# Kernel optimization log

Measured on AMD Instinct MI355X. Metric: run time of the kernel, lower is better.

The kernel has to match this reference:

```python
import jax, jax.numpy as jnp
import numpy as np

C = 768
HEADS = 12
NF = 8      # num_frames
SL = 196    # seq_len (patches per frame)
B = 2
N = 1 + NF * SL
HID = 4 * C


def _ln(x, g, b, eps=1e-5):
    mu = jnp.mean(x, axis=-1, keepdims=True)
    var = jnp.mean((x - mu) ** 2, axis=-1, keepdims=True)
    return (x - mu) * jax.lax.rsqrt(var + eps) * g + b


def setup_inputs() -> dict:
    key = jax.random.key(0)
    ks = jax.random.split(key, 16)
    s = 0.02
    return {
        "x": jax.random.normal(ks[0], (B, N, C), jnp.float32),
        "g1": jnp.ones((C,), jnp.float32),
        "b1": jnp.zeros((C,), jnp.float32),
        "Wqkv": jax.random.normal(ks[1], (C, 3 * C), jnp.float32) * s,
        "Wq": jax.random.normal(ks[2], (C, C), jnp.float32) * s,
        "Wkv": jax.random.normal(ks[3], (C, 2 * C), jnp.float32) * s,
        "Wp": jax.random.normal(ks[4], (C, C), jnp.float32) * s,
        "bp": jnp.zeros((C,), jnp.float32),
        "g2": jnp.ones((C,), jnp.float32),
        "b2": jnp.zeros((C,), jnp.float32),
        "W1": jax.random.normal(ks[5], (C, HID), jnp.float32) * s,
        "bf1": jnp.zeros((HID,), jnp.float32),
        "W2": jax.random.normal(ks[6], (HID, C), jnp.float32) * s,
        "bf2": jnp.zeros((C,), jnp.float32),
        "seq_len": SL,
        "num_frames": NF,
    }


def _traj_attn(xn, Wqkv, Wq, Wkv, Wp, bp, P, F):
    Bb, Nn, Cc = xn.shape
    h = HEADS
    d = Cc // h
    scale = d ** -0.5
    S = F * P  # non-cls tokens

    qkv = xn @ Wqkv                                   # (B,N,3C)
    q, k, v = jnp.split(qkv, 3, axis=-1)

    def heads(t):  # (B,N,C) -> (B*h, N, d)
        return t.reshape(Bb, Nn, h, d).transpose(0, 2, 1, 3).reshape(Bb * h, Nn, d)

    q, k, v = heads(q), heads(k), heads(v)
    cls_q, q_ = q[:, :1], q[:, 1:]
    k_ = k[:, 1:]
    v_ = v[:, 1:]

    # cls token attends to all tokens
    sim = jnp.einsum('bid,bjd->bij', cls_q * scale, k)
    cls_out = jnp.einsum('bij,bjd->bid', jax.nn.softmax(sim, axis=-1), v)
    cls_out = cls_out.reshape(Bb, h, 1, d).transpose(0, 2, 1, 3).reshape(Bb, 1, Cc)

    # stage 1: space-only softmax per frame
    qk = jnp.einsum('bqd,bkd->bqk', q_, k_).reshape(Bb * h, S, F, P)
    space_attn = jax.nn.softmax(scale * qk, axis=-1)          # (Bh,S,F,P)
    v_r = v_.reshape(Bb * h, F, P, d)
    x1 = jnp.einsum('bqfn,bfnd->bqfd', space_attn, v_r)       # (Bh,S,F,d)
    x1 = x1.reshape(Bb, h, S, F, d).transpose(0, 2, 3, 1, 4).reshape(Bb, S, F, Cc)

    # diagonal across (query-frame, key-frame)
    xg = x1.reshape(Bb, F, P, F, Cc)
    diag = jnp.diagonal(xg, axis1=1, axis2=3)                 # (B,P,C,F)
    x_diag = diag.transpose(0, 3, 1, 2).reshape(Bb, S, Cc)    # b (f n) d

    # stage 2: frame-wise attention
    q2 = (x_diag @ Wq).reshape(Bb, S, h, d).transpose(0, 2, 1, 3) * scale  # bhsd
    kv2 = x1 @ Wkv
    k2, v2 = jnp.split(kv2, 2, axis=-1)
    k2 = k2.reshape(Bb, S, F, h, d).transpose(0, 3, 1, 2, 4)  # bhsfd
    attn2 = jax.nn.softmax(jnp.einsum('bhsd,bhsfd->bhsf', q2, k2), axis=-1)
    xo = x1.reshape(Bb, S, F, h, d).transpose(0, 3, 1, 2, 4)  # use_original_code=True
    out = jnp.einsum('bhsf,bhsfd->bhsd', attn2, xo)
    out = out.transpose(0, 2, 1, 3).reshape(Bb, S, Cc)

    out = jnp.concatenate([cls_out, out], axis=1) @ Wp + bp
    return out


def reference(x, g1, b1, Wqkv, Wq, Wkv, Wp, bp, g2, b2, W1, bf1, W2, bf2, seq_len, num_frames):
    x = x + _traj_attn(_ln(x, g1, b1), Wqkv, Wq, Wkv, Wp, bp, seq_len, num_frames)
    h = _ln(x, g2, b2)
    h = jax.nn.gelu(h @ W1 + bf1, approximate=False) @ W2 + bf2
    return x + h
```

## Files before the change

kernel.cpp:

```cpp
#include <hip/hip_runtime.h>
#include <hip/hip_bf16.h>
#include <math.h>

#define C     768
#define HEADS 12
#define HD    64
#define NF    8
#define SL    196
#define BB    2
#define NN    1569
#define SS    1568
#define HID   3072
#define CLS_CH 256
#define CLS_NC 7
#define QSCALE 0.18033688011112042f

typedef __attribute__((ext_vector_type(8))) short short8;
typedef __attribute__((ext_vector_type(4))) float f32x4;
typedef unsigned short u16;

__device__ inline float fast_exp2(float x) { return __builtin_amdgcn_exp2f(x); }

__device__ inline u16 f2b(float f) {
    __hip_bfloat16 h = __float2bfloat16(f);
    return *reinterpret_cast<u16*>(&h);
}
__device__ inline float b2f(u16 u) {
    union { unsigned u; float f; } v; v.u = ((unsigned)u) << 16;
    return v.f;
}

__device__ inline void gload_lds16(const void* g, void* l) {
    __builtin_amdgcn_global_load_lds(
        (const __attribute__((address_space(1))) void*)g,
        (__attribute__((address_space(3))) void*)l, 16, 0, 0);
}

__global__ void ln_kernel(const float* __restrict__ x, const float* __restrict__ g,
                          const float* __restrict__ b, u16* __restrict__ out, int rows) {
    int row = blockIdx.x;
    if (row >= rows) return;
    const float* xr = x + (size_t)row * C;
    int tid = threadIdx.x;
    float v[3];
    float sum = 0.f, sumsq = 0.f;
#pragma unroll
    for (int i = 0; i < 3; i++) {
        v[i] = xr[tid + 256 * i];
        sum += v[i]; sumsq += v[i] * v[i];
    }
    __shared__ float s1[4], s2[4];
    for (int off = 32; off; off >>= 1) {
        sum   += __shfl_xor(sum, off);
        sumsq += __shfl_xor(sumsq, off);
    }
    int wave = tid >> 6, lane = tid & 63;
    if (lane == 0) { s1[wave] = sum; s2[wave] = sumsq; }
    __syncthreads();
    sum   = s1[0] + s1[1] + s1[2] + s1[3];
    sumsq = s2[0] + s2[1] + s2[2] + s2[3];
    float mu  = sum / C;
    float var = sumsq / C - mu * mu;
    float rstd = rsqrtf(fmaxf(var, 0.f) + 1e-5f);
    u16* outr = out + (size_t)row * C;
#pragma unroll
    for (int i = 0; i < 3; i++) {
        int c = tid + 256 * i;
        outr[c] = f2b((v[i] - mu) * rstd * g[c] + b[c]);
    }
}

__global__ void wtrans_all_kernel(
    const float* __restrict__ Wqkv, const float* __restrict__ Wq,
    const float* __restrict__ Wkv,  const float* __restrict__ Wp,
    const float* __restrict__ W1,   const float* __restrict__ W2,
    u16* Tqkv, u16* Tq, u16* Tkv, u16* Tp, u16* T1, u16* T2) {
    __shared__ float tile[64][65];
    int bid = blockIdx.x;
    const float* W; u16* Wt; int K, ldb, gx;
    if (bid < 432)       { W = Wqkv; Wt = Tqkv; K = 768;  ldb = 2304; gx = 36; }
    else if (bid < 576)  { W = Wq;   Wt = Tq;   K = 768;  ldb = 768;  gx = 12; bid -= 432; }
    else if (bid < 720)  { W = Wkv;  Wt = Tkv;  K = 768;  ldb = 1536; gx = 12; bid -= 576; }
    else if (bid < 864)  { W = Wp;   Wt = Tp;   K = 768;  ldb = 768;  gx = 12; bid -= 720; }
    else if (bid < 1440) { W = W1;   Wt = T1;   K = 768;  ldb = 3072; gx = 48; bid -= 864; }
    else                 { W = W2;   Wt = T2;   K = 3072; ldb = 768;  gx = 12; bid -= 1440; }
    int nb = (bid % gx) * 64, kb = (bid / gx) * 64;
    int tx = threadIdx.x & 63, ty = threadIdx.x >> 6;
#pragma unroll
    for (int i = 0; i < 64; i += 4)
        tile[ty + i][tx] = W[(size_t)(kb + ty + i) * ldb + nb + tx];
    __syncthreads();
#pragma unroll
    for (int i = 0; i < 64; i += 4)
        Wt[(size_t)(nb + ty + i) * K + kb + tx] = f2b(tile[tx][ty + i]);
}

template<int MODE, int BM, int BN>
__global__ __launch_bounds__(256) void gemm_bf16(
    const u16* __restrict__ A, const u16* __restrict__ Bt,
    const float* __restrict__ bias, const float* resid, void* Cout,
    int M, int N, int K, int lda, int ldb, int gx) {
    constexpr int MT   = BM / 32;
    constexpr int NT   = BN / 32;
    constexpr int ACH  = BM * 4;
    constexpr int TCH  = (BM + BN) * 4;
    constexpr int HALF = (BM + BN) * 64;
    __shared__ char smem[2 * HALF];
    int tid = threadIdx.x, lane = tid & 63, wave = tid >> 6;
    int wr = wave >> 1, wc = wave & 1;
    int r16 = lane & 15, kg = lane >> 4;

    int nwg = gridDim.x, orig = blockIdx.x;
    int qq = nwg >> 3, rr = nwg & 7, xcd = orig & 7, lid = orig >> 3;
    int wg = (xcd < rr ? xcd * (qq + 1) : rr * (qq + 1) + (xcd - rr) * qq) + lid;
    int bx = wg % gx, by = wg / gx;
    if constexpr (MODE == 4) {
        int mt_ = (M + BM - 1) / BM;
        int chunk = by / mt_; by -= chunk * mt_;
        A    += (size_t)chunk * K;
        Bt   += (size_t)chunk * K;
        Cout  = (void*)((float*)Cout + (size_t)chunk * ((size_t)M * N));
    }
    int row0 = by * BM, col0 = bx * BN;

    f32x4 acc[MT][NT];
#pragma unroll
    for (int mt = 0; mt < MT; mt++)
#pragma unroll
        for (int nt = 0; nt < NT; nt++) acc[mt][nt] = (f32x4){0.f, 0.f, 0.f, 0.f};

    auto stage = [&](char* dstbase, int ks) {
        int k0 = ks << 5;
#pragma unroll
        for (int it = 0; it < TCH / 256; it++) {
            int c = it * 256 + tid;
            const u16* src;
            if (c < ACH) {
                int ml = c >> 2, s = c & 3;
                int kgs = s ^ ((ml >> 1) & 3);
                int gm = row0 + ml; if (gm >= M) gm = M - 1;
                src = A + (size_t)gm * lda + k0 + kgs * 8;
            } else {
                int cc = c - ACH;
                int nl = cc >> 2, s = cc & 3;
                int kgs = s ^ ((nl >> 1) & 3);
                src = Bt + (size_t)(col0 + nl) * ldb + k0 + kgs * 8;
            }
            gload_lds16(src, dstbase + it * 4096 + wave * 1024);
        }
    };

    int nsteps = K >> 5;
    stage(smem, 0);
    __syncthreads();
    for (int ks = 0; ks < nsteps; ks++) {
        char* curb = smem + (ks & 1) * HALF;
        if (ks + 1 < nsteps) stage(smem + ((ks + 1) & 1) * HALF, ks + 1);
        short8 af[MT], bfr[NT];
#pragma unroll
        for (int mt = 0; mt < MT; mt++) {
            int ml = wr * (BM / 2) + mt * 16 + r16;
            af[mt] = *(const short8*)(curb + ml * 64 + ((kg ^ ((ml >> 1) & 3)) << 4));
        }
#pragma unroll
        for (int nt = 0; nt < NT; nt++) {
            int nl = wc * (BN / 2) + nt * 16 + r16;
            bfr[nt] = *(const short8*)(curb + BM * 64 + nl * 64 + ((kg ^ ((nl >> 1) & 3)) << 4));
        }
        __builtin_amdgcn_s_setprio(1);
#pragma unroll
        for (int mt = 0; mt < MT; mt++)
#pragma unroll
            for (int nt = 0; nt < NT; nt++)
                acc[mt][nt] = __builtin_amdgcn_mfma_f32_16x16x32_bf16(af[mt], bfr[nt], acc[mt][nt], 0, 0, 0);
        __builtin_amdgcn_s_setprio(0);
        __syncthreads();
    }
#pragma unroll
    for (int mt = 0; mt < MT; mt++) {
#pragma unroll
        for (int r2 = 0; r2 < 4; r2++) {
            int gm = row0 + wr * (BM / 2) + mt * 16 + kg * 4 + r2;
            if (gm >= M) continue;
#pragma unroll
            for (int nt = 0; nt < NT; nt++) {
                int gn = col0 + wc * (BN / 2) + nt * 16 + r16;
                float v = acc[mt][nt][r2];
                if constexpr (MODE == 1) {
                    v += bias[gn];
                    v = 0.5f * v * (1.f + erff(v * 0.70710678118f));
                }
                if constexpr (MODE == 2) {
                    v += bias[gn] + resid[(size_t)gm * N + gn];
                    ((float*)Cout)[(size_t)gm * N + gn] = v;
                } else if constexpr (MODE == 4) {
                    ((float*)Cout)[(size_t)gm * N + gn] = v;
                } else {
                    if constexpr (MODE == 3) { if (gn < 768) v *= QSCALE; }
                    ((u16*)Cout)[(size_t)gm * N + gn] = f2b(v);
                }
            }
        }
    }
}

__global__ void fc2_merge_kernel(const float* __restrict__ p,
                                 const float* __restrict__ bias, float* __restrict__ out) {
    int i = blockIdx.x * 256 + threadIdx.x;
    int total = BB * NN * (C / 4);
    if (i >= total) return;
    int c4 = i % (C / 4);
    size_t stride = (size_t)BB * NN * (C / 4);
    float4 bb = ((const float4*)bias)[c4];
    float4 a0 = ((const float4*)p)[i];
    float4 a1 = ((const float4*)p)[i + stride];
    float4 a2 = ((const float4*)p)[i + 2 * stride];
    float4 a3 = ((const float4*)p)[i + 3 * stride];
    float4 o  = ((float4*)out)[i];
    o.x += a0.x + a1.x + a2.x + a3.x + bb.x;
    o.y += a0.y + a1.y + a2.y + a3.y + bb.y;
    o.z += a0.z + a1.z + a2.z + a3.z + bb.z;
    o.w += a0.w + a1.w + a2.w + a3.w + bb.w;
    ((float4*)out)[i] = o;
}

__global__ void cls_partial_kernel(const u16* __restrict__ qkv, float* __restrict__ part) {
    int c = blockIdx.x, bh = blockIdx.y;
    int b = bh / HEADS, hh = bh % HEADS;
    int tid = threadIdx.x;
    int wave = tid >> 6, lane = tid & 63;
    __shared__ float s_q[HD];
    __shared__ float s_sc[CLS_CH];
    __shared__ float sm[4], ss[4];
    __shared__ float sacc[4][HD];
    if (tid < HD) s_q[tid] = b2f(qkv[(size_t)(b * NN) * 2304 + hh * HD + tid]);
    __syncthreads();

    int j0 = c * CLS_CH;
    int j = j0 + tid;
    float sc = -1e30f;
    if (j < NN) {
        const short8* kp = (const short8*)(qkv + ((size_t)(b * NN) + j) * 2304 + C + hh * HD);
        float acc = 0.f;
#pragma unroll
        for (int u = 0; u < 8; u++) {
            short8 kv = kp[u];
#pragma unroll
            for (int e = 0; e < 8; e++) acc += s_q[u * 8 + e] * b2f((u16)kv[e]);
        }
        sc = acc;
    }
    float m = sc;
    for (int off = 32; off; off >>= 1) m = fmaxf(m, __shfl_xor(m, off));
    if (lane == 0) sm[wave] = m;
    __syncthreads();
    m = fmaxf(fmaxf(sm[0], sm[1]), fmaxf(sm[2], sm[3]));
    float e = (j < NN) ? fast_exp2(sc - m) : 0.f;
    s_sc[tid] = e;
    float su = e;
    for (int off = 32; off; off >>= 1) su += __shfl_xor(su, off);
    if (lane == 0) ss[wave] = su;
    __syncthreads();
    float ssum = ss[0] + ss[1] + ss[2] + ss[3];

    int jj = tid >> 6, d = tid & 63;
    int jmax = NN - j0; if (jmax > CLS_CH) jmax = CLS_CH;
    const u16* vcol = qkv + ((size_t)(b * NN) + j0) * 2304 + 2 * C + hh * HD + d;
    float acc = 0.f;
    for (int t = jj; t < jmax; t += 4)
        acc += s_sc[t] * b2f(vcol[(size_t)t * 2304]);
    sacc[jj][d] = acc;
    __syncthreads();
    if (tid < HD) {
        float pv = sacc[0][tid] + sacc[1][tid] + sacc[2][tid] + sacc[3][tid];
        float* pp = part + ((size_t)bh * CLS_NC + c) * 66;
        pp[2 + tid] = pv;
        if (tid == 0) { pp[0] = m; pp[1] = ssum; }
    }
}

__global__ void cls_reduce_kernel(const float* __restrict__ part, u16* __restrict__ y) {
    int bh = blockIdx.x;
    int b = bh / HEADS, hh = bh % HEADS;
    int d = threadIdx.x;
    float gm = -1e30f;
#pragma unroll
    for (int c = 0; c < CLS_NC; c++)
        gm = fmaxf(gm, part[((size_t)bh * CLS_NC + c) * 66]);
    float tot = 0.f, pv = 0.f;
#pragma unroll
    for (int c = 0; c < CLS_NC; c++) {
        const float* pp = part + ((size_t)bh * CLS_NC + c) * 66;
        float w = fast_exp2(pp[0] - gm);
        tot += pp[1] * w;
        pv  += pp[2 + d] * w;
    }
    y[(size_t)(b * NN) * C + hh * HD + d] = f2b(pv / tot);
}

__global__ void repack_kv_kernel(const u16* __restrict__ qkv,
                                 u16* __restrict__ Kb, u16* __restrict__ Vt) {
    const int NK = 24 * NF * 208 * 8;
    const int NV = 24 * NF * 64 * 28;
    int t = blockIdx.x * 256 + threadIdx.x;
    if (t < NK) {
        int d8 = t & 7;
        int rest = t >> 3;
        int n = rest % 208;
        rest /= 208;
        int f = rest % NF;
        int bh = rest / NF;
        int b = bh / HEADS, h = bh % HEADS;
        short8 v = {0, 0, 0, 0, 0, 0, 0, 0};
        if (n < SL)
            v = *(const short8*)(qkv + ((size_t)(b * NN) + 1 + f * SL + n) * 2304 + C + h * HD + d8 * 8);
        *(short8*)(Kb + (((size_t)bh * NF + f) * 208 + n) * 64 + d8 * 8) = v;
    } else {
        int u = t - NK;
        if (u >= NV) return;
        int n8 = u % 28;
        int rest = u / 28;
        int d = rest % 64;
        rest /= 64;
        int f = rest % NF;
        int bh = rest / NF;
        int b = bh / HEADS, h = bh % HEADS;
        int n0 = n8 * 8;
        const u16* src = qkv + ((size_t)(b * NN) + 1 + f * SL) * 2304 + 2 * C + h * HD + d;
        short8 v;
#pragma unroll
        for (int jj = 0; jj < 8; jj++) {
            int n = n0 + jj;
            v[jj] = (n < SL) ? (short)src[(size_t)n * 2304] : (short)0;
        }
        *(short8*)(Vt + (((size_t)bh * NF + f) * 64 + d) * 224 + n0) = v;
    }
}

__global__ void space_attn_mfma(
    const u16* __restrict__ qkv, const u16* __restrict__ Kb,
    const u16* __restrict__ Vt, u16* __restrict__ x1, u16* __restrict__ xd) {
    __shared__ u16 smem[14848];
    int tid = threadIdx.x;
    int lane = tid & 63, wave = tid >> 6;
    int r16 = lane & 15, kg = lane >> 4;

    int n = blockIdx.x;
    int xcd = n & 7;
    int slot = n >> 3;
    int j = slot % 25;
    int gw = slot / 25;
    int bh = xcd * 3 + gw % 3;
    int f = gw / 3;
    int b = bh / HEADS, h = bh % HEADS;

    int strip = j * 4 + wave;
    bool act = strip < 98;
    if (!act) strip = 97;
    int q0 = strip * 16;

    const u16* qrow = qkv + ((size_t)(b * NN) + 1 + q0 + r16) * 2304 + h * HD + kg * 8;
    short8 aq0 = *(const short8*)(qrow);
    short8 aq1 = *(const short8*)(qrow + 32);

    const char* kb_g = (const char*)(Kb + ((size_t)bh * NF + f) * 208 * 64);
    for (int w = wave; w < 26; w += 4) {
        int p = w * 1024 + lane * 16;
        int row = p >> 7;
        int src = (p & ~127) | ((p & 127) ^ ((row & 7) << 4));
        gload_lds16(kb_g + src, (char*)smem + p);
    }
    __syncthreads();

    f32x4 acc[13];
#pragma unroll
    for (int t = 0; t < 13; t++) acc[t] = (f32x4){0.f, 0.f, 0.f, 0.f};
    const char* ksm = (const char*)smem;
    int swz = (r16 & 7) << 4;
    __builtin_amdgcn_s_setprio(1);
#pragma unroll
    for (int t = 0; t < 13; t++) {
        const char* krow = ksm + (t * 16 + r16) * 128;
        short8 bk0 = *(const short8*)(krow + ((kg * 16) ^ swz));
        short8 bk1 = *(const short8*)(krow + ((64 + kg * 16) ^ swz));
        acc[t] = __builtin_amdgcn_mfma_f32_16x16x32_bf16(aq0, bk0, acc[t], 0, 0, 0);
        acc[t] = __builtin_amdgcn_mfma_f32_16x16x32_bf16(aq1, bk1, acc[t], 0, 0, 0);
    }
    __builtin_amdgcn_s_setprio(0);

    const u16* vbase = Vt + ((size_t)bh * NF + f) * 64 * 224;
    short8 vf[2][4];
#pragma unroll
    for (int dt = 0; dt < 4; dt++)
        vf[0][dt] = *(const short8*)(vbase + (dt * 16 + r16) * 224 + kg * 8);

    __syncthreads();
    u16* pb = smem + wave * 3712;

    bool tail_mask = (r16 >= 4);
    float ssum[4] = {0.f, 0.f, 0.f, 0.f};
#pragma unroll
    for (int t = 0; t < 13; t++) {
#pragma unroll
        for (int r = 0; r < 4; r++) {
            float p = (t == 12 && tail_mask) ? 0.f : fast_exp2(acc[t][r]);
            ssum[r] += p;
            pb[(kg * 4 + r) * 232 + t * 16 + r16] = f2b(p);
        }
    }
    {
        int zr = lane >> 2, zc = 208 + (lane & 3) * 4;
        *(uint2*)(&pb[zr * 232 + zc]) = (uint2){0u, 0u};
    }
#pragma unroll
    for (int off = 8; off; off >>= 1)
#pragma unroll
        for (int r = 0; r < 4; r++) ssum[r] += __shfl_xor(ssum[r], off);
    float inv[4];
#pragma unroll
    for (int r = 0; r < 4; r++) inv[r] = 1.f / ssum[r];

    f32x4 o[4];
#pragma unroll
    for (int dt = 0; dt < 4; dt++) o[dt] = (f32x4){0.f, 0.f, 0.f, 0.f};
    __builtin_amdgcn_s_setprio(1);
#pragma unroll
    for (int kc = 0; kc < 7; kc++) {
        if (kc < 6) {
#pragma unroll
            for (int dt = 0; dt < 4; dt++)
                vf[(kc + 1) & 1][dt] = *(const short8*)(vbase + (dt * 16 + r16) * 224 + (kc + 1) * 32 + kg * 8);
        }
        short8 pa = *(const short8*)(&pb[r16 * 232 + kc * 32 + kg * 8]);
#pragma unroll
        for (int dt = 0; dt < 4; dt++)
            o[dt] = __builtin_amdgcn_mfma_f32_16x16x32_bf16(pa, vf[kc & 1][dt], o[dt], 0, 0, 0);
    }
    __builtin_amdgcn_s_setprio(0);

    if (act) {
#pragma unroll
        for (int dt = 0; dt < 4; dt++)
#pragma unroll
            for (int r = 0; r < 4; r++)
                pb[(kg * 4 + r) * 72 + dt * 16 + r16] = f2b(o[dt][r] * inv[r]);
        u16* x1row = x1 + (((size_t)(b * SS + q0)) * NF + f) * C + h * HD;
        u16* xdrow = xd + ((size_t)(b * SS + q0)) * C + h * HD;
        int fbase = f * SL;
#pragma unroll
        for (int it = 0; it < 2; it++) {
            int c = it * 64 + lane;
            int qr = c >> 3, c8 = c & 7;
            short8 v8 = *(const short8*)(&pb[qr * 72 + c8 * 8]);
            *(short8*)(x1row + (size_t)qr * (NF * C) + c8 * 8) = v8;
            if ((unsigned)(q0 + qr - fbase) < (unsigned)SL)
                *(short8*)(xdrow + (size_t)qr * C + c8 * 8) = v8;
        }
    }
}

__global__ void attn2_kernel(const u16* __restrict__ q2, const u16* __restrict__ k2,
                             const u16* __restrict__ x1, u16* __restrict__ y) {
    int item = blockIdx.x * 4 + (threadIdx.x >> 6);
    if (item >= BB * HEADS * SS) return;
    int lane = threadIdx.x & 63;
    int s = item % SS;
    int bh = item / SS;
    int b = bh / HEADS, hh = bh % HEADS;
    size_t rowbs = (size_t)(b * SS + s);
    float qv = b2f(q2[rowbs * C + hh * HD + lane]) * QSCALE;
    float lg[NF];
#pragma unroll
    for (int f = 0; f < NF; f++) {
        float p = qv * b2f(k2[(rowbs * NF + f) * C + hh * HD + lane]);
        for (int off = 32; off; off >>= 1) p += __shfl_xor(p, off);
        lg[f] = p;
    }
    float m = lg[0];
#pragma unroll
    for (int f = 1; f < NF; f++) m = fmaxf(m, lg[f]);
    float sum = 0.f;
#pragma unroll
    for (int f = 0; f < NF; f++) { lg[f] = fast_exp2(lg[f] - m); sum += lg[f]; }
    float inv = 1.f / sum;
    float acc = 0.f;
#pragma unroll
    for (int f = 0; f < NF; f++) acc += lg[f] * b2f(x1[(rowbs * NF + f) * C + hh * HD + lane]);
    y[((size_t)(b * NN) + 1 + s) * C + hh * HD + lane] = f2b(acc * inv);
}

extern "C" void kernel_launch(void* const* d_in, const int* in_sizes, int n_in,
                              void* d_out, int out_size, void* d_ws, size_t ws_size,
                              hipStream_t stream) {
    const float* x    = (const float*)d_in[0];
    const float* g1   = (const float*)d_in[1];
    const float* b1   = (const float*)d_in[2];
    const float* Wqkv = (const float*)d_in[3];
    const float* Wq   = (const float*)d_in[4];
    const float* Wkv  = (const float*)d_in[5];
    const float* Wp   = (const float*)d_in[6];
    const float* bp   = (const float*)d_in[7];
    const float* g2   = (const float*)d_in[8];
    const float* b2_  = (const float*)d_in[9];
    const float* W1   = (const float*)d_in[10];
    const float* bf1  = (const float*)d_in[11];
    const float* W2   = (const float*)d_in[12];
    const float* bf2  = (const float*)d_in[13];
    float* out = (float*)d_out;

    u16* us     = (u16*)d_ws;
    u16* xn_b   = us;
    u16* qkv_b  = xn_b   + 2409984;
    u16* Wt_qkv = qkv_b  + 7229952;
    u16* Wt_q   = Wt_qkv + 1769472;
    u16* Wt_kv  = Wt_q   + 589824;
    u16* Wt_p   = Wt_kv  + 589824;
    u16* W1t    = Wt_p   + 589824;
    u16* W2t    = W1t    + 2359296;
    u16* Kb     = W2t    + 2359296;
    u16* Vt     = Kb     + 2555904;
    u16* x1b    = Vt     + 2752512;
    u16* xdb    = x1b    + 19267584;
    u16* q2b    = xdb    + 2408448;
    u16* k2b    = q2b    + 2408448;
    u16* y_b    = k2b    + 19267584;
    u16* a1b    = y_b    + 2409984;
    float* cls_ws   = (float*)(a1b + 9639936);
    float* fc2_part = cls_ws + 24 * 7 * 66;

    const int M1 = BB * NN;
    const int M2 = BB * SS;
    const int M3 = BB * SS * NF;

    wtrans_all_kernel<<<2016, 256, 0, stream>>>(Wqkv, Wq, Wkv, Wp, W1, W2,
                                                Wt_qkv, Wt_q, Wt_kv, Wt_p, W1t, W2t);
    ln_kernel<<<M1, 256, 0, stream>>>(x, g1, b1, xn_b, M1);
    gemm_bf16<3, 128, 64><<<36 * 25, 256, 0, stream>>>(
        xn_b, Wt_qkv, nullptr, nullptr, qkv_b, M1, 2304, 768, 768, 768, 36);
    repack_kv_kernel<<<(24 * NF * 208 * 8 + 24 * NF * 64 * 28 + 255) / 256, 256, 0, stream>>>(
        qkv_b, Kb, Vt);
    cls_partial_kernel<<<dim3(CLS_NC, BB * HEADS), 256, 0, stream>>>(qkv_b, cls_ws);
    cls_reduce_kernel<<<BB * HEADS, 64, 0, stream>>>(cls_ws, y_b);
    space_attn_mfma<<<4800, 256, 0, stream>>>(qkv_b, Kb, Vt, x1b, xdb);
    gemm_bf16<0, 64, 64><<<12 * 49, 256, 0, stream>>>(
        xdb, Wt_q, nullptr, nullptr, q2b, M2, 768, 768, 768, 768, 12);
    gemm_bf16<0, 128, 128><<<6 * 196, 256, 0, stream>>>(
        x1b, Wt_kv, nullptr, nullptr, k2b, M3, 768, 768, 768, 768, 6);
    attn2_kernel<<<(BB * HEADS * SS + 3) / 4, 256, 0, stream>>>(q2b, k2b, x1b, y_b);
    gemm_bf16<2, 64, 64><<<12 * 50, 256, 0, stream>>>(
        y_b, Wt_p, bp, x, out, M1, 768, 768, 768, 768, 12);
    ln_kernel<<<M1, 256, 0, stream>>>(out, g2, b2_, xn_b, M1);
    gemm_bf16<1, 128, 64><<<48 * 25, 256, 0, stream>>>(
        xn_b, W1t, bf1, nullptr, a1b, M1, 3072, 768, 768, 768, 48);
    gemm_bf16<4, 128, 64><<<12 * 25 * 4, 256, 0, stream>>>(
        a1b, W2t, nullptr, nullptr, fc2_part, M1, 768, 768, 3072, 3072, 12);
    fc2_merge_kernel<<<(BB * NN * (C / 4) + 255) / 256, 256, 0, stream>>>(
        fc2_part, bf2, out);
}
```

Before: 295.7 us.

## Transpose space-attn QK MFMA to store P row-contiguous; halve fc2 split-K

The space-attention kernel swaps the MFMA operand order so each lane holds scores for one query row across keys. This lets the row sum reduce with two cross-lane shuffles instead of per-register butterflies, and P is normalized before packed 8-byte stores to LDS instead of scattered 2-byte stores. Separately, the FC2 GEMM split-K factor drops from 4 to 2, so the merge kernel reads two partial buffers instead of four. The cost is fewer FC2 blocks for parallelism and more live registers for the stored exponentials.

```diff
diff --git a/kernel.cpp b/kernel.cpp
--- a/kernel.cpp
+++ b/kernel.cpp
@@ -18,6 +18,7 @@
 typedef __attribute__((ext_vector_type(8))) short short8;
 typedef __attribute__((ext_vector_type(4))) float f32x4;
 typedef unsigned short u16;
+typedef unsigned int u32;
 
 __device__ inline float fast_exp2(float x) { return __builtin_amdgcn_exp2f(x); }
 
@@ -214,13 +215,11 @@
     float4 bb = ((const float4*)bias)[c4];
     float4 a0 = ((const float4*)p)[i];
     float4 a1 = ((const float4*)p)[i + stride];
-    float4 a2 = ((const float4*)p)[i + 2 * stride];
-    float4 a3 = ((const float4*)p)[i + 3 * stride];
     float4 o  = ((float4*)out)[i];
-    o.x += a0.x + a1.x + a2.x + a3.x + bb.x;
-    o.y += a0.y + a1.y + a2.y + a3.y + bb.y;
-    o.z += a0.z + a1.z + a2.z + a3.z + bb.z;
-    o.w += a0.w + a1.w + a2.w + a3.w + bb.w;
+    o.x += a0.x + a1.x + bb.x;
+    o.y += a0.y + a1.y + bb.y;
+    o.z += a0.z + a1.z + bb.z;
+    o.w += a0.w + a1.w + bb.w;
     ((float4*)out)[i] = o;
 }
 
@@ -383,8 +382,8 @@
         const char* krow = ksm + (t * 16 + r16) * 128;
         short8 bk0 = *(const short8*)(krow + ((kg * 16) ^ swz));
         short8 bk1 = *(const short8*)(krow + ((64 + kg * 16) ^ swz));
-        acc[t] = __builtin_amdgcn_mfma_f32_16x16x32_bf16(aq0, bk0, acc[t], 0, 0, 0);
-        acc[t] = __builtin_amdgcn_mfma_f32_16x16x32_bf16(aq1, bk1, acc[t], 0, 0, 0);
+        acc[t] = __builtin_amdgcn_mfma_f32_16x16x32_bf16(bk0, aq0, acc[t], 0, 0, 0);
+        acc[t] = __builtin_amdgcn_mfma_f32_16x16x32_bf16(bk1, aq1, acc[t], 0, 0, 0);
     }
     __builtin_amdgcn_s_setprio(0);
 
@@ -397,28 +396,32 @@
     __syncthreads();
     u16* pb = smem + wave * 3712;
 
-    bool tail_mask = (r16 >= 4);
-    float ssum[4] = {0.f, 0.f, 0.f, 0.f};
+    bool tailz = (kg >= 1);
+    float ssum = 0.f;
+    float pv_[13][4];
 #pragma unroll
     for (int t = 0; t < 13; t++) {
 #pragma unroll
         for (int r = 0; r < 4; r++) {
-            float p = (t == 12 && tail_mask) ? 0.f : fast_exp2(acc[t][r]);
-            ssum[r] += p;
-            pb[(kg * 4 + r) * 232 + t * 16 + r16] = f2b(p);
-        }
+            float p = (t == 12 && tailz) ? 0.f : fast_exp2(acc[t][r]);
+            pv_[t][r] = p;
+            ssum += p;
+        }
+    }
+    ssum += __shfl_xor(ssum, 16);
+    ssum += __shfl_xor(ssum, 32);
+    float inv = 1.f / ssum;
+
+#pragma unroll
+    for (int t = 0; t < 13; t++) {
+        u32 w0 = (u32)f2b(pv_[t][0] * inv) | ((u32)f2b(pv_[t][1] * inv) << 16);
+        u32 w1 = (u32)f2b(pv_[t][2] * inv) | ((u32)f2b(pv_[t][3] * inv) << 16);
+        *(uint2*)(&pb[r16 * 232 + t * 16 + kg * 4]) = (uint2){w0, w1};
     }
     {
         int zr = lane >> 2, zc = 208 + (lane & 3) * 4;
         *(uint2*)(&pb[zr * 232 + zc]) = (uint2){0u, 0u};
     }
-#pragma unroll
-    for (int off = 8; off; off >>= 1)
-#pragma unroll
-        for (int r = 0; r < 4; r++) ssum[r] += __shfl_xor(ssum[r], off);
-    float inv[4];
-#pragma unroll
-    for (int r = 0; r < 4; r++) inv[r] = 1.f / ssum[r];
 
     f32x4 o[4];
 #pragma unroll
@@ -443,7 +446,7 @@
         for (int dt = 0; dt < 4; dt++)
 #pragma unroll
             for (int r = 0; r < 4; r++)
-                pb[(kg * 4 + r) * 72 + dt * 16 + r16] = f2b(o[dt][r] * inv[r]);
+                pb[(kg * 4 + r) * 72 + dt * 16 + r16] = f2b(o[dt][r]);
         u16* x1row = x1 + (((size_t)(b * SS + q0)) * NF + f) * C + h * HD;
         u16* xdrow = xd + ((size_t)(b * SS + q0)) * C + h * HD;
         int fbase = f * SL;
@@ -552,8 +555,8 @@
     ln_kernel<<<M1, 256, 0, stream>>>(out, g2, b2_, xn_b, M1);
     gemm_bf16<1, 128, 64><<<48 * 25, 256, 0, stream>>>(
         xn_b, W1t, bf1, nullptr, a1b, M1, 3072, 768, 768, 768, 48);
-    gemm_bf16<4, 128, 64><<<12 * 25 * 4, 256, 0, stream>>>(
-        a1b, W2t, nullptr, nullptr, fc2_part, M1, 768, 768, 3072, 3072, 12);
+    gemm_bf16<4, 128, 64><<<12 * 25 * 2, 256, 0, stream>>>(
+        a1b, W2t, nullptr, nullptr, fc2_part, M1, 768, 1536, 3072, 3072, 12);
     fc2_merge_kernel<<<(BB * NN * (C / 4) + 255) / 256, 256, 0, stream>>>(
         fc2_part, bf2, out);
 }
```

Result: no change. 291.8 us, median of 2 (-1.3%).
